# Kernel optimization log

Measured on AMD Instinct MI355X. Metric: run time of the kernel, lower is better.

## Reference

```python
import jax, jax.numpy as jnp
import numpy as np


def setup_inputs() -> dict:
    key = jax.random.key(0)
    ks = jax.random.split(key, 7)
    B, T, D = 4, 4096, 128
    s = 0.02
    return {
        "input_data": jax.random.normal(ks[0], (B, T, D), dtype=jnp.float32),
        "Wq": jax.random.normal(ks[1], (D, D), dtype=jnp.float32) * s,
        "bq": jax.random.normal(ks[2], (D,), dtype=jnp.float32) * s,
        "Wk": jax.random.normal(ks[3], (D, D), dtype=jnp.float32) * s,
        "bk": jax.random.normal(ks[4], (D,), dtype=jnp.float32) * s,
        "Wv": jax.random.normal(ks[5], (D, D), dtype=jnp.float32) * s,
        "bv": jax.random.normal(ks[6], (D,), dtype=jnp.float32) * s,
    }


def reference(input_data, Wq, bq, Wk, bk, Wv, bv):
    D = input_data.shape[-1]
    scale = jnp.asarray(D, input_data.dtype) ** 0.5
    # torch Linear: x @ W.T + b
    q = input_data @ Wq.T + bq  # [B,T,D]
    k = input_data @ Wk.T + bk
    v = input_data @ Wv.T + bv
    energy = jnp.einsum("btd,bsd->bts", q, k) / scale  # [B,T,T]
    attn = jax.nn.softmax(energy, axis=-1)
    return jnp.einsum("bts,bsd->btd", attn, v)  # [B,T,D]
```

## Files before the change

kernel.cpp:

```cpp
#include <hip/hip_runtime.h>
#include <cstdint>

typedef _Float16 half2_t __attribute__((ext_vector_type(2)));
typedef _Float16 half4_t __attribute__((ext_vector_type(4)));
typedef _Float16 half8_t __attribute__((ext_vector_type(8)));
typedef float floatx4 __attribute__((ext_vector_type(4)));

#define T_SEQ 4096
#define D_HEAD 128
#define SCALE_LOG2 0.12751742526f

__device__ __forceinline__ void gload16(const void* src, void* dst_lds) {
    using gptr_t = const __attribute__((address_space(1))) unsigned int*;
    using lptr_t = __attribute__((address_space(3))) unsigned int*;
    __builtin_amdgcn_global_load_lds((gptr_t)(uintptr_t)src,
                                     (lptr_t)(unsigned int)(uintptr_t)dst_lds, 16, 0, 0);
}

__global__ __launch_bounds__(256) void proj_kernel(
    const float* __restrict__ x,
    const float* __restrict__ Wq, const float* __restrict__ bq,
    const float* __restrict__ Wk, const float* __restrict__ bk,
    const float* __restrict__ Wv, const float* __restrict__ bv,
    _Float16* __restrict__ qf, _Float16* __restrict__ kf, _Float16* __restrict__ vt)
{
    __shared__ __align__(16) _Float16 Ws[128 * 136];
    __shared__ __align__(16) _Float16 xs[64 * 136];

    const int t = threadIdx.x;
    const int mat = blockIdx.y;
    const float* W = (mat == 0) ? Wq : (mat == 1) ? Wk : Wv;
    const float* bias = (mat == 0) ? bq : (mat == 1) ? bk : bv;
    const float osc = (mat == 0) ? SCALE_LOG2 : 1.0f;
    const int r0 = blockIdx.x * 64;

    {
        const int o = t >> 1;
        const int i0 = (t & 1) * 64;
        for (int jj = 0; jj < 8; ++jj) {
            floatx4 w0 = *reinterpret_cast<const floatx4*>(W + o * 128 + i0 + jj * 8);
            floatx4 w1 = *reinterpret_cast<const floatx4*>(W + o * 128 + i0 + jj * 8 + 4);
            half8_t h;
            h[0]=(_Float16)w0[0]; h[1]=(_Float16)w0[1]; h[2]=(_Float16)w0[2]; h[3]=(_Float16)w0[3];
            h[4]=(_Float16)w1[0]; h[5]=(_Float16)w1[1]; h[6]=(_Float16)w1[2]; h[7]=(_Float16)w1[3];
            *reinterpret_cast<half8_t*>(&Ws[o * 136 + i0 + jj * 8]) = h;
        }
    }
    {
        const int row = t >> 2;
        const int c0 = (t & 3) * 32;
        for (int jj = 0; jj < 4; ++jj) {
            floatx4 w0 = *reinterpret_cast<const floatx4*>(x + (size_t)(r0 + row) * 128 + c0 + jj * 8);
            floatx4 w1 = *reinterpret_cast<const floatx4*>(x + (size_t)(r0 + row) * 128 + c0 + jj * 8 + 4);
            half8_t h;
            h[0]=(_Float16)w0[0]; h[1]=(_Float16)w0[1]; h[2]=(_Float16)w0[2]; h[3]=(_Float16)w0[3];
            h[4]=(_Float16)w1[0]; h[5]=(_Float16)w1[1]; h[6]=(_Float16)w1[2]; h[7]=(_Float16)w1[3];
            *reinterpret_cast<half8_t*>(&xs[row * 136 + c0 + jj * 8]) = h;
        }
    }
    __syncthreads();

    const int w = t >> 6;
    const int lane = t & 63;
    const int lo = lane & 15, hi = lane >> 4;

    floatx4 acc[8] = {};
    for (int dc = 0; dc < 4; ++dc) {
        half8_t a8 = *reinterpret_cast<const half8_t*>(&xs[(w * 16 + lo) * 136 + dc * 32 + hi * 8]);
        for (int ot = 0; ot < 8; ++ot) {
            half8_t b8 = *reinterpret_cast<const half8_t*>(&Ws[(ot * 16 + lo) * 136 + dc * 32 + hi * 8]);
            acc[ot] = __builtin_amdgcn_mfma_f32_16x16x32_f16(a8, b8, acc[ot], 0, 0, 0);
        }
    }
    __syncthreads();

    float bb[8];
    for (int ot = 0; ot < 8; ++ot) bb[ot] = bias[ot * 16 + lo];

    if (mat < 2) {
        _Float16* ol = xs;
        for (int ot = 0; ot < 8; ++ot)
            for (int r = 0; r < 4; ++r)
                ol[(w * 16 + hi * 4 + r) * 136 + ot * 16 + lo] = (_Float16)((acc[ot][r] + bb[ot]) * osc);
        __syncthreads();
        _Float16* dst = (mat == 0) ? qf : kf;
        for (int i = 0; i < 4; ++i) {
            int c = t + 256 * i;
            int row = c >> 4, p = c & 15;
            half8_t v = *reinterpret_cast<const half8_t*>(&ol[row * 136 + p * 8]);
            *reinterpret_cast<half8_t*>(dst + (size_t)(r0 + row) * 128 + p * 8) = v;
        }
    } else {
        _Float16* vl = Ws;
        for (int ot = 0; ot < 8; ++ot)
            for (int r = 0; r < 4; ++r)
                vl[(ot * 16 + lo) * 72 + w * 16 + hi * 4 + r] = (_Float16)(acc[ot][r] + bb[ot]);
        __syncthreads();
        const int b = r0 >> 12, tl0 = r0 & 4095;
        for (int i = 0; i < 4; ++i) {
            int c = t + 256 * i;
            int d = c >> 3, p = c & 7;
            half8_t v = *reinterpret_cast<const half8_t*>(&vl[d * 72 + p * 8]);
            *reinterpret_cast<half8_t*>(vt + ((size_t)(b * 128 + d)) * 4096 + tl0 + p * 8) = v;
        }
    }
}

__global__ __launch_bounds__(512, 1) void attn_kernel(
    const _Float16* __restrict__ qf, const _Float16* __restrict__ kf,
    const _Float16* __restrict__ vt, float* __restrict__ out)
{
    __shared__ __align__(16) char smem[131072];

    const int tid = threadIdx.x;
    const int w = tid >> 6, lane = tid & 63;
    const int lo = lane & 15, hi = lane >> 4;
    const int qt2 = w & 1, split = w >> 1;

    const int bx = blockIdx.x;
    const int wg = (bx & 7) * 32 + (bx >> 3);
    const int b = wg >> 6;
    const int q0 = (wg & 63) * 64;

    const char* kbc = (const char*)(kf + (size_t)b * T_SEQ * 128);
    const char* vbc = (const char*)(vt + (size_t)b * 128 * T_SEQ);

    int koff[4], kdst[4];
#pragma unroll
    for (int r = 0; r < 4; ++r) {
        int seg = w * 4 + r;
        int slot = lane & 15;
        int row = seg * 4 + (lane >> 4);
        koff[r] = row * 256 + ((slot ^ (row & 7)) << 4);
        kdst[r] = seg * 1024 + lane * 16;
    }

    const int vc = tid & 15;
    const int vua = ((vc >> 2) << 2) + ((vc & 1) << 1);
    const int voffb = (vc & 2) << 2;
    int vgo[4], vwa[4], vwb[4];
#pragma unroll
    for (int i = 0; i < 4; ++i) {
        int d = (tid >> 4) + 32 * i;
        vgo[i] = d * (T_SEQ * 2) + vc * 16;
        vwa[i] = 32768 + d * 256 + (((vua)     ^ (d & 7)) << 4) + voffb;
        vwb[i] = 32768 + d * 256 + (((vua + 1) ^ (d & 7)) << 4) + voffb;
    }

    int kro[2][4];
#pragma unroll
    for (int s = 0; s < 2; ++s)
#pragma unroll
        for (int dc = 0; dc < 4; ++dc)
            kro[s][dc] = (split * 32 + s * 16 + lo) * 256 + ((((dc * 4 + hi)) ^ (lo & 7)) << 4);
    int vro[8];
#pragma unroll
    for (int dt = 0; dt < 8; ++dt)
        vro[dt] = 32768 + (dt * 16 + lo) * 256 + (((split * 4 + hi) ^ (lo & 7)) << 4);

    half8_t qfrag[2][4];
#pragma unroll
    for (int qt = 0; qt < 2; ++qt) {
        const _Float16* qrow = qf + ((size_t)b * T_SEQ + q0 + qt2 * 32 + qt * 16 + lo) * 128;
#pragma unroll
        for (int dc = 0; dc < 4; ++dc)
            qfrag[qt][dc] = *reinterpret_cast<const half8_t*>(qrow + dc * 32 + hi * 8);
    }

    floatx4 accO[2][8] = {};
    float m_run[2] = {-1e30f, -1e30f}, l_run[2] = {0.f, 0.f};

#pragma unroll
    for (int r = 0; r < 4; ++r) gload16(kbc + koff[r], smem + kdst[r]);
    {
        uint4 vreg[4];
#pragma unroll
        for (int i = 0; i < 4; ++i) vreg[i] = *reinterpret_cast<const uint4*>(vbc + vgo[i]);
#pragma unroll
        for (int i = 0; i < 4; ++i) {
            *reinterpret_cast<uint2*>(smem + vwa[i]) = make_uint2(vreg[i].x, vreg[i].y);
            *reinterpret_cast<uint2*>(smem + vwb[i]) = make_uint2(vreg[i].z, vreg[i].w);
        }
    }
    __syncthreads();

#define TILE(T0, CUR, NXT, PF) do {                                                    \
    uint4 vreg[4];                                                                     \
    if (PF) {                                                                          \
        const char* vs = vbc + (size_t)((T0) + 128) * 2;                               \
        _Pragma("unroll")                                                              \
        for (int i = 0; i < 4; ++i)                                                    \
            vreg[i] = *reinterpret_cast<const uint4*>(vs + vgo[i]);                    \
        const char* ks = kbc + (size_t)((T0) + 128) * 256;                             \
        _Pragma("unroll")                                                              \
        for (int r = 0; r < 4; ++r) gload16(ks + koff[r], smem + (NXT) + kdst[r]);     \
    }                                                                                  \
    const char* bufc = smem + (CUR);                                                   \
    floatx4 sac[2][2] = {};                                                            \
    __builtin_amdgcn_s_setprio(1);                                                     \
    _Pragma("unroll")                                                                  \
    for (int s = 0; s < 2; ++s) {                                                      \
        _Pragma("unroll")                                                              \
        for (int dc = 0; dc < 4; ++dc) {                                               \
            half8_t kf8 = *reinterpret_cast<const half8_t*>(bufc + kro[s][dc]);        \
            sac[0][s] = __builtin_amdgcn_mfma_f32_16x16x32_f16(kf8, qfrag[0][dc], sac[0][s], 0, 0, 0); \
            sac[1][s] = __builtin_amdgcn_mfma_f32_16x16x32_f16(kf8, qfrag[1][dc], sac[1][s], 0, 0, 0); \
        }                                                                              \
    }                                                                                  \
    __builtin_amdgcn_s_setprio(0);                                                     \
    float bm[2];                                                                       \
    bool ok = true;                                                                    \
    _Pragma("unroll")                                                                  \
    for (int qt = 0; qt < 2; ++qt) {                                                   \
        float m0 = fmaxf(fmaxf(sac[qt][0][0], sac[qt][0][1]), fmaxf(sac[qt][0][2], sac[qt][0][3])); \
        float m1 = fmaxf(fmaxf(sac[qt][1][0], sac[qt][1][1]), fmaxf(sac[qt][1][2], sac[qt][1][3])); \
        float m = fmaxf(m0, m1);                                                       \
        m = fmaxf(m, __shfl_xor(m, 16));                                               \
        m = fmaxf(m, __shfl_xor(m, 32));                                               \
        bm[qt] = m;                                                                    \
        ok = ok && (m <= m_run[qt] + 4.0f);                                            \
    }                                                                                  \
    if (!__all(ok)) {                                                                  \
        _Pragma("unroll")                                                              \
        for (int qt = 0; qt < 2; ++qt) {                                               \
            float m_new = fmaxf(m_run[qt], bm[qt]);                                    \
            float alpha = exp2f(m_run[qt] - m_new);                                    \
            l_run[qt] *= alpha;                                                        \
            _Pragma("unroll")                                                          \
            for (int dt = 0; dt < 8; ++dt) accO[qt][dt] *= alpha;                      \
            m_run[qt] = m_new;                                                         \
        }                                                                              \
    }                                                                                  \
    half8_t pa[2];                                                                     \
    _Pragma("unroll")                                                                  \
    for (int qt = 0; qt < 2; ++qt) {                                                   \
        float pv[8];                                                                   \
        float bs = 0.f;                                                                \
        _Pragma("unroll")                                                              \
        for (int j = 0; j < 8; ++j) {                                                  \
            int s = j >> 2, r = j & 3;                                                 \
            pv[j] = exp2f(sac[qt][s][r] - m_run[qt]);                                  \
            bs += pv[j];                                                               \
        }                                                                              \
        bs += __shfl_xor(bs, 16);                                                      \
        bs += __shfl_xor(bs, 32);                                                      \
        l_run[qt] += bs;                                                               \
        _Pragma("unroll")                                                              \
        for (int j2 = 0; j2 < 4; ++j2) {                                               \
            half2_t h2 = __builtin_bit_cast(half2_t,                                   \
                __builtin_amdgcn_cvt_pkrtz(pv[j2 * 2], pv[j2 * 2 + 1]));               \
            pa[qt][j2 * 2] = h2[0];                                                    \
            pa[qt][j2 * 2 + 1] = h2[1];                                                \
        }                                                                              \
    }                                                                                  \
    __builtin_amdgcn_s_setprio(1);                                                     \
    _Pragma("unroll")                                                                  \
    for (int dt = 0; dt < 8; ++dt) {                                                   \
        half8_t vfr = *reinterpret_cast<const half8_t*>(bufc + vro[dt]);               \
        accO[0][dt] = __builtin_amdgcn_mfma_f32_16x16x32_f16(vfr, pa[0], accO[0][dt], 0, 0, 0); \
        accO[1][dt] = __builtin_amdgcn_mfma_f32_16x16x32_f16(vfr, pa[1], accO[1][dt], 0, 0, 0); \
    }                                                                                  \
    __builtin_amdgcn_s_setprio(0);                                                     \
    if (PF) {                                                                          \
        _Pragma("unroll")                                                              \
        for (int i = 0; i < 4; ++i) {                                                  \
            *reinterpret_cast<uint2*>(smem + (NXT) + vwa[i]) = make_uint2(vreg[i].x, vreg[i].y); \
            *reinterpret_cast<uint2*>(smem + (NXT) + vwb[i]) = make_uint2(vreg[i].z, vreg[i].w); \
        }                                                                              \
    }                                                                                  \
    __syncthreads();                                                                   \
} while (0)

    for (int t0 = 0; t0 < T_SEQ; t0 += 256) {
        TILE(t0, 0, 65536, true);
        TILE(t0 + 128, 65536, 0, (t0 + 256 < T_SEQ));
    }
#undef TILE

    float* red_m = reinterpret_cast<float*>(smem + 40960);
    float* red_l = reinterpret_cast<float*>(smem + 43008);
    int row64[2]; float fac[2];
#pragma unroll
    for (int qt = 0; qt < 2; ++qt) row64[qt] = qt2 * 32 + qt * 16 + lo;
    if (hi == 0) {
#pragma unroll
        for (int qt = 0; qt < 2; ++qt) {
            red_m[split * 64 + row64[qt]] = m_run[qt];
            red_l[split * 64 + row64[qt]] = l_run[qt];
        }
    }
    __syncthreads();
#pragma unroll
    for (int qt = 0; qt < 2; ++qt) {
        float M = -1e30f;
#pragma unroll
        for (int s = 0; s < 4; ++s) M = fmaxf(M, red_m[s * 64 + row64[qt]]);
        float L = 0.f;
#pragma unroll
        for (int s = 0; s < 4; ++s) L += red_l[s * 64 + row64[qt]] * exp2f(red_m[s * 64 + row64[qt]] - M);
        fac[qt] = exp2f(m_run[qt] - M) / L;
    }
    float* out_lds = reinterpret_cast<float*>(smem);
    for (int s = 0; s < 4; ++s) {
        if (split == s) {
#pragma unroll
            for (int qt = 0; qt < 2; ++qt)
#pragma unroll
                for (int dt = 0; dt < 8; ++dt)
#pragma unroll
                    for (int r = 0; r < 4; ++r) {
                        int d = dt * 16 + hi * 4 + r;
                        float v = accO[qt][dt][r] * fac[qt];
                        float* p = &out_lds[row64[qt] * 132 + d];
                        if (s == 0) *p = v; else *p += v;
                    }
        }
        __syncthreads();
    }
    {
        int row = tid >> 3, d0 = (tid & 7) * 16;
        float* op = out + ((size_t)b * T_SEQ + q0 + row) * 128 + d0;
#pragma unroll
        for (int j = 0; j < 4; ++j) {
            float4 v;
            v.x = out_lds[row * 132 + d0 + j * 4 + 0];
            v.y = out_lds[row * 132 + d0 + j * 4 + 1];
            v.z = out_lds[row * 132 + d0 + j * 4 + 2];
            v.w = out_lds[row * 132 + d0 + j * 4 + 3];
            *reinterpret_cast<float4*>(op + j * 4) = v;
        }
    }
}

extern "C" void kernel_launch(void* const* d_in, const int* in_sizes, int n_in,
                              void* d_out, int out_size, void* d_ws, size_t ws_size,
                              hipStream_t stream)
{
    (void)in_sizes; (void)n_in; (void)out_size; (void)ws_size;
    const float* x  = (const float*)d_in[0];
    const float* Wq = (const float*)d_in[1];
    const float* bq = (const float*)d_in[2];
    const float* Wk = (const float*)d_in[3];
    const float* bk = (const float*)d_in[4];
    const float* Wv = (const float*)d_in[5];
    const float* bv = (const float*)d_in[6];
    float* out = (float*)d_out;

    _Float16* qf = (_Float16*)d_ws;
    _Float16* kf = qf + (size_t)4 * T_SEQ * D_HEAD;
    _Float16* vt = kf + (size_t)4 * T_SEQ * D_HEAD;

    proj_kernel<<<dim3(256, 3), 256, 0, stream>>>(x, Wq, bq, Wk, bk, Wv, bv, qf, kf, vt);
    attn_kernel<<<dim3(256), 512, 0, stream>>>(qf, kf, vt, out);
}
```

Baseline: 85.29 us.

## Restructure attention split: 8-way key split per wave with software-pipelined PV

Each of the 8 waves now owns a 16-key slice of every tile and computes scores for all 64 queries, instead of splitting waves into query halves and 4 key splits. The P·V MFMA for the previous tile is deferred and overlapped with the QK of the current tile, and uses 16x16x16 MFMAs with per-wave V fragments. The per-tile max reduction across lanes is skipped unless a rescale is needed, raw exp2 intrinsics replace exp2f, and the V global-to-LDS copy becomes a single 16-byte store. The cost is more accumulator registers (4x8 floatx4), an extra barrier per tile, and an 8-way final cross-wave reduction.

```diff
diff --git a/kernel.cpp b/kernel.cpp
--- a/kernel.cpp
+++ b/kernel.cpp
@@ -15,6 +15,14 @@
     using lptr_t = __attribute__((address_space(3))) unsigned int*;
     __builtin_amdgcn_global_load_lds((gptr_t)(uintptr_t)src,
                                      (lptr_t)(unsigned int)(uintptr_t)dst_lds, 16, 0, 0);
+}
+
+__device__ __forceinline__ float exp2_raw(float x) {
+#if __has_builtin(__builtin_amdgcn_exp2f)
+    return __builtin_amdgcn_exp2f(x);
+#else
+    return exp2f(x);
+#endif
 }
 
 __global__ __launch_bounds__(256) void proj_kernel(
@@ -115,7 +123,6 @@
     const int tid = threadIdx.x;
     const int w = tid >> 6, lane = tid & 63;
     const int lo = lane & 15, hi = lane >> 4;
-    const int qt2 = w & 1, split = w >> 1;
 
     const int bx = blockIdx.x;
     const int wg = (bx & 7) * 32 + (bx >> 3);
@@ -134,184 +141,173 @@
         koff[r] = row * 256 + ((slot ^ (row & 7)) << 4);
         kdst[r] = seg * 1024 + lane * 16;
     }
-
-    const int vc = tid & 15;
-    const int vua = ((vc >> 2) << 2) + ((vc & 1) << 1);
-    const int voffb = (vc & 2) << 2;
-    int vgo[4], vwa[4], vwb[4];
+    const int vd = tid >> 2, vq = tid & 3;
+    int vglob[4], vwds[4];
 #pragma unroll
     for (int i = 0; i < 4; ++i) {
-        int d = (tid >> 4) + 32 * i;
-        vgo[i] = d * (T_SEQ * 2) + vc * 16;
-        vwa[i] = 32768 + d * 256 + (((vua)     ^ (d & 7)) << 4) + voffb;
-        vwb[i] = 32768 + d * 256 + (((vua + 1) ^ (d & 7)) << 4) + voffb;
-    }
-
-    int kro[2][4];
-#pragma unroll
-    for (int s = 0; s < 2; ++s)
-#pragma unroll
-        for (int dc = 0; dc < 4; ++dc)
-            kro[s][dc] = (split * 32 + s * 16 + lo) * 256 + ((((dc * 4 + hi)) ^ (lo & 7)) << 4);
+        int c = vq * 4 + i;
+        vglob[i] = vd * (T_SEQ * 2) + c * 16;
+        vwds[i] = 32768 + vd * 256 + ((c ^ (vd & 7)) << 4);
+    }
+    int kro[4];
+#pragma unroll
+    for (int dc = 0; dc < 4; ++dc)
+        kro[dc] = (w * 16 + lo) * 256 + (((dc * 4 + hi) ^ (lo & 7)) << 4);
     int vro[8];
 #pragma unroll
     for (int dt = 0; dt < 8; ++dt)
-        vro[dt] = 32768 + (dt * 16 + lo) * 256 + (((split * 4 + hi) ^ (lo & 7)) << 4);
-
-    half8_t qfrag[2][4];
-#pragma unroll
-    for (int qt = 0; qt < 2; ++qt) {
-        const _Float16* qrow = qf + ((size_t)b * T_SEQ + q0 + qt2 * 32 + qt * 16 + lo) * 128;
+        vro[dt] = 32768 + (dt * 16 + lo) * 256 +
+                  (((w * 2 + (hi >> 1)) ^ (lo & 7)) << 4) + ((hi & 1) << 3);
+
+    half8_t qfrag[4][4];
+#pragma unroll
+    for (int qt = 0; qt < 4; ++qt) {
+        const _Float16* qrow = qf + ((size_t)b * T_SEQ + q0 + qt * 16 + lo) * 128;
 #pragma unroll
         for (int dc = 0; dc < 4; ++dc)
             qfrag[qt][dc] = *reinterpret_cast<const half8_t*>(qrow + dc * 32 + hi * 8);
     }
 
-    floatx4 accO[2][8] = {};
-    float m_run[2] = {-1e30f, -1e30f}, l_run[2] = {0.f, 0.f};
+    floatx4 accO[4][8] = {};
+    float m[4] = {-1e30f, -1e30f, -1e30f, -1e30f};
+    float l[4] = {};
+    half4_t pa[4] = {};
 
 #pragma unroll
     for (int r = 0; r < 4; ++r) gload16(kbc + koff[r], smem + kdst[r]);
-    {
-        uint4 vreg[4];
-#pragma unroll
-        for (int i = 0; i < 4; ++i) vreg[i] = *reinterpret_cast<const uint4*>(vbc + vgo[i]);
-#pragma unroll
-        for (int i = 0; i < 4; ++i) {
-            *reinterpret_cast<uint2*>(smem + vwa[i]) = make_uint2(vreg[i].x, vreg[i].y);
-            *reinterpret_cast<uint2*>(smem + vwb[i]) = make_uint2(vreg[i].z, vreg[i].w);
-        }
-    }
-    __syncthreads();
-
-#define TILE(T0, CUR, NXT, PF) do {                                                    \
-    uint4 vreg[4];                                                                     \
+#pragma unroll
+    for (int i = 0; i < 4; ++i) {
+        uint4 v = *reinterpret_cast<const uint4*>(vbc + vglob[i]);
+        *reinterpret_cast<uint4*>(smem + vwds[i]) = v;
+    }
+    __syncthreads();
+
+#define TILE(T0, CUR, NXT, PF, DOPREV) do {                                            \
+    uint4 vr[4];                                                                       \
     if (PF) {                                                                          \
+        const char* ks = kbc + (size_t)((T0) + 128) * 256;                             \
+        _Pragma("unroll")                                                              \
+        for (int r = 0; r < 4; ++r) gload16(ks + koff[r], smem + (NXT) + kdst[r]);     \
         const char* vs = vbc + (size_t)((T0) + 128) * 2;                               \
         _Pragma("unroll")                                                              \
         for (int i = 0; i < 4; ++i)                                                    \
-            vreg[i] = *reinterpret_cast<const uint4*>(vs + vgo[i]);                    \
-        const char* ks = kbc + (size_t)((T0) + 128) * 256;                             \
-        _Pragma("unroll")                                                              \
-        for (int r = 0; r < 4; ++r) gload16(ks + koff[r], smem + (NXT) + kdst[r]);     \
-    }                                                                                  \
-    const char* bufc = smem + (CUR);                                                   \
-    floatx4 sac[2][2] = {};                                                            \
+            vr[i] = *reinterpret_cast<const uint4*>(vs + vglob[i]);                    \
+    }                                                                                  \
+    floatx4 sac[4] = {};                                                               \
     __builtin_amdgcn_s_setprio(1);                                                     \
     _Pragma("unroll")                                                                  \
-    for (int s = 0; s < 2; ++s) {                                                      \
-        _Pragma("unroll")                                                              \
-        for (int dc = 0; dc < 4; ++dc) {                                               \
-            half8_t kf8 = *reinterpret_cast<const half8_t*>(bufc + kro[s][dc]);        \
-            sac[0][s] = __builtin_amdgcn_mfma_f32_16x16x32_f16(kf8, qfrag[0][dc], sac[0][s], 0, 0, 0); \
-            sac[1][s] = __builtin_amdgcn_mfma_f32_16x16x32_f16(kf8, qfrag[1][dc], sac[1][s], 0, 0, 0); \
+    for (int dc = 0; dc < 4; ++dc) {                                                   \
+        half8_t kf8 = *reinterpret_cast<const half8_t*>(smem + (CUR) + kro[dc]);       \
+        _Pragma("unroll")                                                              \
+        for (int qt = 0; qt < 4; ++qt)                                                 \
+            sac[qt] = __builtin_amdgcn_mfma_f32_16x16x32_f16(kf8, qfrag[qt][dc], sac[qt], 0, 0, 0); \
+    }                                                                                  \
+    __builtin_amdgcn_s_setprio(0);                                                     \
+    bool ok = true;                                                                    \
+    float mp[4];                                                                       \
+    _Pragma("unroll")                                                                  \
+    for (int qt = 0; qt < 4; ++qt) {                                                   \
+        mp[qt] = fmaxf(fmaxf(sac[qt][0], sac[qt][1]), fmaxf(sac[qt][2], sac[qt][3]));  \
+        ok = ok && (mp[qt] <= m[qt] + 4.0f);                                           \
+    }                                                                                  \
+    if (!__all(ok)) {                                                                  \
+        _Pragma("unroll")                                                              \
+        for (int qt = 0; qt < 4; ++qt) {                                               \
+            float r = mp[qt];                                                          \
+            r = fmaxf(r, __shfl_xor(r, 16)); r = fmaxf(r, __shfl_xor(r, 32));          \
+            float n = fmaxf(m[qt], r);                                                 \
+            float a = exp2_raw(m[qt] - n);                                             \
+            l[qt] *= a;                                                                \
+            _Pragma("unroll")                                                          \
+            for (int dt = 0; dt < 8; ++dt) accO[qt][dt] *= a;                          \
+            m[qt] = n;                                                                 \
         }                                                                              \
     }                                                                                  \
-    __builtin_amdgcn_s_setprio(0);                                                     \
-    float bm[2];                                                                       \
-    bool ok = true;                                                                    \
+    if (DOPREV) {                                                                      \
+        __builtin_amdgcn_s_setprio(1);                                                 \
+        _Pragma("unroll")                                                              \
+        for (int dt = 0; dt < 8; ++dt) {                                               \
+            half4_t vfr = *reinterpret_cast<const half4_t*>(smem + (NXT) + vro[dt]);   \
+            _Pragma("unroll")                                                          \
+            for (int qt = 0; qt < 4; ++qt)                                             \
+                accO[qt][dt] = __builtin_amdgcn_mfma_f32_16x16x16f16(vfr, pa[qt], accO[qt][dt], 0, 0, 0); \
+        }                                                                              \
+        __builtin_amdgcn_s_setprio(0);                                                 \
+    }                                                                                  \
+    __syncthreads();               \
+    if (PF) {                                                                          \
+        _Pragma("unroll")                                                              \
+        for (int i = 0; i < 4; ++i)                                                    \
+            *reinterpret_cast<uint4*>(smem + (NXT) + vwds[i]) = vr[i];                 \
+    }                                                                                  \
     _Pragma("unroll")                                                                  \
-    for (int qt = 0; qt < 2; ++qt) {                                                   \
-        float m0 = fmaxf(fmaxf(sac[qt][0][0], sac[qt][0][1]), fmaxf(sac[qt][0][2], sac[qt][0][3])); \
-        float m1 = fmaxf(fmaxf(sac[qt][1][0], sac[qt][1][1]), fmaxf(sac[qt][1][2], sac[qt][1][3])); \
-        float m = fmaxf(m0, m1);                                                       \
-        m = fmaxf(m, __shfl_xor(m, 16));                                               \
-        m = fmaxf(m, __shfl_xor(m, 32));                                               \
-        bm[qt] = m;                                                                    \
-        ok = ok && (m <= m_run[qt] + 4.0f);                                            \
-    }                                                                                  \
-    if (!__all(ok)) {                                                                  \
-        _Pragma("unroll")                                                              \
-        for (int qt = 0; qt < 2; ++qt) {                                               \
-            float m_new = fmaxf(m_run[qt], bm[qt]);                                    \
-            float alpha = exp2f(m_run[qt] - m_new);                                    \
-            l_run[qt] *= alpha;                                                        \
-            _Pragma("unroll")                                                          \
-            for (int dt = 0; dt < 8; ++dt) accO[qt][dt] *= alpha;                      \
-            m_run[qt] = m_new;                                                         \
-        }                                                                              \
-    }                                                                                  \
-    half8_t pa[2];                                                                     \
-    _Pragma("unroll")                                                                  \
-    for (int qt = 0; qt < 2; ++qt) {                                                   \
-        float pv[8];                                                                   \
-        float bs = 0.f;                                                                \
-        _Pragma("unroll")                                                              \
-        for (int j = 0; j < 8; ++j) {                                                  \
-            int s = j >> 2, r = j & 3;                                                 \
-            pv[j] = exp2f(sac[qt][s][r] - m_run[qt]);                                  \
-            bs += pv[j];                                                               \
-        }                                                                              \
-        bs += __shfl_xor(bs, 16);                                                      \
-        bs += __shfl_xor(bs, 32);                                                      \
-        l_run[qt] += bs;                                                               \
-        _Pragma("unroll")                                                              \
-        for (int j2 = 0; j2 < 4; ++j2) {                                               \
-            half2_t h2 = __builtin_bit_cast(half2_t,                                   \
-                __builtin_amdgcn_cvt_pkrtz(pv[j2 * 2], pv[j2 * 2 + 1]));               \
-            pa[qt][j2 * 2] = h2[0];                                                    \
-            pa[qt][j2 * 2 + 1] = h2[1];                                                \
-        }                                                                              \
-    }                                                                                  \
-    __builtin_amdgcn_s_setprio(1);                                                     \
-    _Pragma("unroll")                                                                  \
-    for (int dt = 0; dt < 8; ++dt) {                                                   \
-        half8_t vfr = *reinterpret_cast<const half8_t*>(bufc + vro[dt]);               \
-        accO[0][dt] = __builtin_amdgcn_mfma_f32_16x16x32_f16(vfr, pa[0], accO[0][dt], 0, 0, 0); \
-        accO[1][dt] = __builtin_amdgcn_mfma_f32_16x16x32_f16(vfr, pa[1], accO[1][dt], 0, 0, 0); \
-    }                                                                                  \
-    __builtin_amdgcn_s_setprio(0);                                                     \
-    if (PF) {                                                                          \
-        _Pragma("unroll")                                                              \
-        for (int i = 0; i < 4; ++i) {                                                  \
-            *reinterpret_cast<uint2*>(smem + (NXT) + vwa[i]) = make_uint2(vreg[i].x, vreg[i].y); \
-            *reinterpret_cast<uint2*>(smem + (NXT) + vwb[i]) = make_uint2(vreg[i].z, vreg[i].w); \
-        }                                                                              \
-    }                                                                                  \
-    __syncthreads();                                                                   \
+    for (int qt = 0; qt < 4; ++qt) {                                                   \
+        float p0 = exp2_raw(sac[qt][0] - m[qt]), p1 = exp2_raw(sac[qt][1] - m[qt]);    \
+        float p2 = exp2_raw(sac[qt][2] - m[qt]), p3 = exp2_raw(sac[qt][3] - m[qt]);    \
+        l[qt] += (p0 + p1) + (p2 + p3);                                                \
+        half2_t h0 = __builtin_bit_cast(half2_t, __builtin_amdgcn_cvt_pkrtz(p0, p1));  \
+        half2_t h1 = __builtin_bit_cast(half2_t, __builtin_amdgcn_cvt_pkrtz(p2, p3));  \
+        pa[qt][0] = h0[0]; pa[qt][1] = h0[1]; pa[qt][2] = h1[0]; pa[qt][3] = h1[1];    \
+    }                                                                                  \
+    __syncthreads();        \
 } while (0)
 
-    for (int t0 = 0; t0 < T_SEQ; t0 += 256) {
-        TILE(t0, 0, 65536, true);
-        TILE(t0 + 128, 65536, 0, (t0 + 256 < T_SEQ));
-    }
+    TILE(0, 0, 65536, 1, 0);
+    for (int tt = 128; tt < 3840; tt += 256) {
+        TILE(tt,       65536, 0,     1, 1);
+        TILE(tt + 128, 0,     65536, 1, 1);
+    }
+    TILE(3968, 65536, 0, 0, 1);
 #undef TILE
 
-    float* red_m = reinterpret_cast<float*>(smem + 40960);
-    float* red_l = reinterpret_cast<float*>(smem + 43008);
-    int row64[2]; float fac[2];
-#pragma unroll
-    for (int qt = 0; qt < 2; ++qt) row64[qt] = qt2 * 32 + qt * 16 + lo;
+#pragma unroll
+    for (int dt = 0; dt < 8; ++dt) {
+        half4_t vfr = *reinterpret_cast<const half4_t*>(smem + 65536 + vro[dt]);
+#pragma unroll
+        for (int qt = 0; qt < 4; ++qt)
+            accO[qt][dt] = __builtin_amdgcn_mfma_f32_16x16x16f16(vfr, pa[qt], accO[qt][dt], 0, 0, 0);
+    }
+
+#pragma unroll
+    for (int qt = 0; qt < 4; ++qt) {
+        l[qt] += __shfl_xor(l[qt], 16);
+        l[qt] += __shfl_xor(l[qt], 32);
+    }
+
+    float* red_m = reinterpret_cast<float*>(smem + 65536);
+    float* red_l = reinterpret_cast<float*>(smem + 67584);
+    __syncthreads();
     if (hi == 0) {
 #pragma unroll
-        for (int qt = 0; qt < 2; ++qt) {
-            red_m[split * 64 + row64[qt]] = m_run[qt];
-            red_l[split * 64 + row64[qt]] = l_run[qt];
-        }
-    }
-    __syncthreads();
-#pragma unroll
-    for (int qt = 0; qt < 2; ++qt) {
-        float M = -1e30f;
-#pragma unroll
-        for (int s = 0; s < 4; ++s) M = fmaxf(M, red_m[s * 64 + row64[qt]]);
-        float L = 0.f;
-#pragma unroll
-        for (int s = 0; s < 4; ++s) L += red_l[s * 64 + row64[qt]] * exp2f(red_m[s * 64 + row64[qt]] - M);
-        fac[qt] = exp2f(m_run[qt] - M) / L;
+        for (int qt = 0; qt < 4; ++qt) {
+            red_m[w * 64 + qt * 16 + lo] = m[qt];
+            red_l[w * 64 + qt * 16 + lo] = l[qt];
+        }
+    }
+    __syncthreads();
+    float fac[4];
+#pragma unroll
+    for (int qt = 0; qt < 4; ++qt) {
+        int row = qt * 16 + lo;
+        float M = -1e30f, L = 0.f;
+#pragma unroll
+        for (int s = 0; s < 8; ++s) M = fmaxf(M, red_m[s * 64 + row]);
+#pragma unroll
+        for (int s = 0; s < 8; ++s) L += red_l[s * 64 + row] * exp2_raw(red_m[s * 64 + row] - M);
+        fac[qt] = exp2_raw(m[qt] - M) / L;
     }
     float* out_lds = reinterpret_cast<float*>(smem);
-    for (int s = 0; s < 4; ++s) {
-        if (split == s) {
-#pragma unroll
-            for (int qt = 0; qt < 2; ++qt)
+    for (int s = 0; s < 8; ++s) {
+        if (w == s) {
+#pragma unroll
+            for (int qt = 0; qt < 4; ++qt)
 #pragma unroll
                 for (int dt = 0; dt < 8; ++dt)
 #pragma unroll
                     for (int r = 0; r < 4; ++r) {
                         int d = dt * 16 + hi * 4 + r;
                         float v = accO[qt][dt][r] * fac[qt];
-                        float* p = &out_lds[row64[qt] * 132 + d];
+                        float* p = &out_lds[(qt * 16 + lo) * 132 + d];
                         if (s == 0) *p = v; else *p += v;
                     }
         }
```

New measurement: 220.9 us. 159% more time.
